# Kernel optimization log

Measured on AMD Instinct MI355X. Metric: run time of the kernel, lower is better.

Reference implementation:

```python
import jax, jax.numpy as jnp
import numpy as np

B, S, HID = 2, 2048, 2048
H, D = 16, 128  # heads, head_dim == kernel_hidden_size
GATE_NORM = 16.0
CLAMP_MIN = -50.0


def gla(q, k, v, gk):
    # fused_recurrent_gla: S_t = diag(exp(gk_t)) S_{t-1} + k_t^T v_t; o_t = (q_t*scale) @ S_t
    # q,k,v,gk: [B,H,S,D]
    scale = D ** -0.5
    qs = jnp.moveaxis(q, 2, 0) * scale  # [S,B,H,D]
    ks = jnp.moveaxis(k, 2, 0)
    vs = jnp.moveaxis(v, 2, 0)
    gs = jnp.moveaxis(gk, 2, 0)

    def step(state, xs):
        q_t, k_t, v_t, g_t = xs  # each [B,H,D]
        state = state * jnp.exp(g_t)[..., None] + k_t[..., None] * v_t[..., None, :]
        o_t = jnp.einsum('bhk,bhkv->bhv', q_t, state)
        return state, o_t

    init = jnp.zeros((q.shape[0], H, D, D), q.dtype)
    _, out = jax.lax.scan(step, init, (qs, ks, vs, gs))
    return jnp.moveaxis(out, 0, 2)  # [B,H,S,D]


def setup_inputs() -> dict:
    key = jax.random.key(0)
    ks = jax.random.split(key, 8)
    std = 0.02
    hidden_states = jax.random.normal(ks[0], (B, S, HID), jnp.float32)
    Wq = jax.random.normal(ks[1], (HID, HID), jnp.float32) * std
    Wk = jax.random.normal(ks[2], (HID, HID), jnp.float32) * std
    Wv = jax.random.normal(ks[3], (HID, HID), jnp.float32) * std
    Wo = jax.random.normal(ks[4], (HID, HID), jnp.float32) * std
    Wg1 = jnp.eye(HID, dtype=jnp.float32)  # nn.init.eye_
    bg1 = jnp.zeros((HID,), jnp.float32)
    Wg2 = jnp.eye(HID, dtype=jnp.float32)
    bg2 = jnp.zeros((HID,), jnp.float32)
    alpha_list = jax.random.uniform(ks[5], (2,), jnp.float32)
    return dict(hidden_states=hidden_states, Wq=Wq, Wk=Wk, Wv=Wv, Wo=Wo,
                Wg1=Wg1, bg1=bg1, Wg2=Wg2, bg2=bg2, alpha_list=alpha_list)


def reference(hidden_states, Wq, Wk, Wv, Wo, Wg1, bg1, Wg2, bg2, alpha_list):
    b, s, _ = hidden_states.shape

    def split_heads(x):  # [b,s,hid] -> [b,h,s,d]
        return x.reshape(b, s, H, D).transpose(0, 2, 1, 3)

    q = split_heads(hidden_states @ Wq.T)
    k = split_heads(hidden_states @ Wk.T)
    v = split_heads(hidden_states @ Wv.T)

    def gate(Wg, bg):
        g = split_heads(hidden_states @ Wg.T + bg)
        g = jax.nn.log_sigmoid(g) / GATE_NORM
        return jnp.maximum(g, CLAMP_MIN)

    gk = gate(Wg1, bg1)
    gk2 = gate(Wg2, bg2)

    o1 = gla(q, k, v, gk)
    o2 = gla(q, k, v, gk2)

    a = jax.nn.softmax(alpha_list)
    attn = a[0] * o1 + a[1] * o2  # [b,h,s,d]
    attn = attn.transpose(0, 2, 1, 3).reshape(b, s, HID)
    return attn @ Wo.T
```

## Files before the change

kernel.cpp:

```cpp
#include <hip/hip_runtime.h>
#include <cstdint>
#include <cstddef>


#define BB     2
#define SEQ    2048
#define HIDN   2048
#define NH     16
#define DD     128
#define CHUNK  64
#define NCHUNK (SEQ / CHUNK)
#define NBH    (BB * NH)
#define NELC   8388608
#define WELC   4194304
static constexpr float QSCALE = 0.08838834764831845f;

typedef __bf16 bf16_t;
typedef _Float16 half_t;
typedef short  short8 __attribute__((ext_vector_type(8)));
typedef float  f32x4  __attribute__((ext_vector_type(4)));

__device__ __forceinline__ float bf2f(short u) {
  return (float)__builtin_bit_cast(bf16_t, u);
}
__device__ __forceinline__ short f2bf(float f) {
  return __builtin_bit_cast(short, (bf16_t)f);
}
__device__ __forceinline__ float hf2f(short u) {
  return (float)__builtin_bit_cast(half_t, u);
}
__device__ __forceinline__ short f2hf(float f) {
  return __builtin_bit_cast(short, (half_t)f);
}

__device__ __forceinline__ void gload_lds16(const void* g, void* l) {
  __builtin_amdgcn_global_load_lds(
      (__attribute__((address_space(1))) unsigned int*)g,
      (__attribute__((address_space(3))) unsigned int*)l, 16, 0, 0);
}

#define WVM4 asm volatile("s_waitcnt vmcnt(4)" ::: "memory")
#define WVM2 asm volatile("s_waitcnt vmcnt(2)" ::: "memory")
#define WVM0 asm volatile("s_waitcnt vmcnt(0)" ::: "memory")
#define SBAR __builtin_amdgcn_s_barrier()


#define STG_A(buf, kt, p)                                                   \
  {                                                                         \
    const size_t ko = (size_t)(kt) * 64;                                    \
    gload_lds16(Ag + (size_t)((p) * 64) * HIDN + ko,                        \
                (void*)&As[buf][((p) * 64 + wave * 8) * 64]);               \
    gload_lds16(Ag + (size_t)((p) * 64 + 128) * HIDN + ko,                  \
                (void*)&As[buf][((p) * 64 + 128 + wave * 8) * 64]);         \
  }

#define STG_B(buf, kt, p)                                                   \
  {                                                                         \
    const int cb0 = (wave >> 2) * 64 + (p) * 32 + (wave & 3) * 8;           \
    const size_t ko = (size_t)(kt) * 64;                                    \
    gload_lds16(Bg + (size_t)cb0 * HIDN + ko,                               \
                (void*)&Bs[buf][cb0 * 64]);                                 \
    gload_lds16(Bg + (size_t)(cb0 + 128) * HIDN + ko,                       \
                (void*)&Bs[buf][(cb0 + 128) * 64]);                         \
  }

#define LDA(mh, rb)                                                         \
  {                                                                         \
    _Pragma("unroll") for (int f = 0; f < 4; f++) {                         \
      const int row = wm * 128 + (mh) * 64 + f * 16 + l16;                  \
      af[f][0] = *(const short8*)&As[rb][row * 64 + ((qd ^ ro) << 3)];      \
      af[f][1] =                                                            \
          *(const short8*)&As[rb][row * 64 + (((4 + qd) ^ ro) << 3)];       \
    }                                                                       \
  }

#define LDB2(j0, rb)                                                        \
  {                                                                         \
    _Pragma("unroll") for (int g = 0; g < 2; g++) {                         \
      const int col = wn * 64 + ((j0) + g) * 16 + l16;                      \
      bfr[(j0) + g][0] =                                                    \
          *(const short8*)&Bs[rb][col * 64 + ((qd ^ ro) << 3)];             \
      bfr[(j0) + g][1] =                                                    \
          *(const short8*)&Bs[rb][col * 64 + (((4 + qd) ^ ro) << 3)];       \
    }                                                                       \
  }

#define MQ(mh, nh)                                                          \
  {                                                                         \
    __builtin_amdgcn_s_setprio(1);                                          \
    _Pragma("unroll") for (int ks = 0; ks < 2; ks++)                        \
    _Pragma("unroll") for (int f = 0; f < 4; f++)                           \
    _Pragma("unroll") for (int g = 0; g < 2; g++)                           \
      acc[(mh) * 4 + f][(nh) * 2 + g] =                                     \
          __builtin_amdgcn_mfma_f32_16x16x32_bf16(                          \
              af[f][ks], bfr[(nh) * 2 + g][ks],                             \
              acc[(mh) * 4 + f][(nh) * 2 + g], 0, 0, 0);                    \
    __builtin_amdgcn_s_setprio(0);                                          \
  }

__device__ __forceinline__ void gemm256(const bf16_t* __restrict__ A,
                                        const bf16_t* __restrict__ Bw,
                                        const float*  __restrict__ bias,
                                        bf16_t* __restrict__ outb,
                                        float*  __restrict__ outf, int epi) {
  __shared__ short As[2][256 * 64];
  __shared__ short Bs[2][256 * 64];
  const int tm   = blockIdx.x * 256;
  const int tn   = blockIdx.y * 256;
  const int tid  = threadIdx.x;
  const int wave = tid >> 6;
  const int lane = tid & 63;
  const int wm   = wave >> 2;
  const int wn   = wave & 3;
  const int qd   = lane >> 4;
  const int l16  = lane & 15;
  const int ro   = l16 & 7;
  const int gc   = (lane & 7) ^ (lane >> 3);

  const short* Ag =
      (const short*)A + (size_t)(tm + wave * 8 + (lane >> 3)) * HIDN + gc * 8;
  const short* Bg =
      (const short*)Bw + (size_t)(tn + (lane >> 3)) * HIDN + gc * 8;

  f32x4 acc[8][4];
#pragma unroll
  for (int i = 0; i < 8; i++)
#pragma unroll
    for (int j = 0; j < 4; j++) acc[i][j] = (f32x4){0.f, 0.f, 0.f, 0.f};
  short8 af[4][2], bfr[4][2];

  STG_A(0, 0, 0); STG_B(0, 0, 0); STG_B(0, 0, 1); STG_A(0, 0, 1);
  WVM0;
  SBAR;

  for (int t = 0; t < 32; t++) {
    const int cur = t & 1, nx = cur ^ 1;
    LDA(0, cur);
    LDB2(0, cur);
    if (t < 31) { STG_A(nx, t + 1, 0); }
    MQ(0, 0);
    if (t < 31) { WVM4; } else { WVM2; }
    SBAR;
    LDB2(2, cur);
    if (t < 31) { STG_B(nx, t + 1, 0); }
    MQ(0, 1);
    if (t < 31) { WVM4; } else { WVM0; }
    SBAR;
    LDA(1, cur);
    if (t < 31) { STG_B(nx, t + 1, 1); }
    MQ(1, 1);
    if (t < 31) { STG_A(nx, t + 1, 1); }
    MQ(1, 0);
    if (t < 31) {
      WVM4;
      SBAR;
    }
  }

#pragma unroll
  for (int i = 0; i < 8; i++)
#pragma unroll
    for (int j = 0; j < 4; j++)
#pragma unroll
      for (int r = 0; r < 4; r++) {
        const int row =
            tm + wm * 128 + (i >> 2) * 64 + (i & 3) * 16 + qd * 4 + r;
        const int col = tn + wn * 64 + j * 16 + l16;
        float v = acc[i][j][r];
        if (epi == 1) {
          v += bias[col];
          const float ls = fminf(v, 0.f) - log1pf(__expf(-fabsf(v)));
          v = fmaxf(ls * 0.0625f, -50.f);
        }
        if (epi == 2) outf[(size_t)row * HIDN + col] = v;
        else          outb[(size_t)row * HIDN + col] = (bf16_t)v;
      }
}

__global__ __launch_bounds__(512, 2) void k_gemm_proj(
    const bf16_t* __restrict__ Xb,
    const bf16_t* __restrict__ W0, const bf16_t* __restrict__ W1,
    const bf16_t* __restrict__ W2, const bf16_t* __restrict__ W3,
    const bf16_t* __restrict__ W4,
    const float* __restrict__ bg1, const float* __restrict__ bg2,
    bf16_t* __restrict__ Qb, bf16_t* __restrict__ Kb, bf16_t* __restrict__ Vb,
    bf16_t* __restrict__ G1b, bf16_t* __restrict__ G2b) {
  const int z = blockIdx.z;
  const bf16_t* Ws[5] = {W0, W1, W2, W3, W4};
  bf16_t* Os[5] = {Qb, Kb, Vb, G1b, G2b};
  const float* bias = (z == 3) ? bg1 : ((z == 4) ? bg2 : nullptr);
  gemm256(Xb, Ws[z], bias, Os[z], nullptr, (z >= 3) ? 1 : 0);
}

__global__ __launch_bounds__(512, 2) void k_gemm_out(
    const bf16_t* __restrict__ attnB, const bf16_t* __restrict__ Wob,
    float* __restrict__ out) {
  gemm256(attnB, Wob, nullptr, nullptr, out, 2);
}

__global__ __launch_bounds__(256) void k_cvt_all(
    const float* __restrict__ hid, const float* __restrict__ wq,
    const float* __restrict__ wk, const float* __restrict__ wv,
    const float* __restrict__ wg1, const float* __restrict__ wg2,
    const float* __restrict__ wo, bf16_t* __restrict__ Xb,
    bf16_t* __restrict__ Wd, bf16_t* __restrict__ Wcur,
    bf16_t* __restrict__ WoB) {
  const int y = blockIdx.y;
  const float* srcs[7] = {hid, wq, wk, wv, wg1, wg2, wo};
  bf16_t* dsts[7] = {Xb, Wd, Wd + WELC, Wd + 2 * WELC, Wd + 3 * WELC, Wcur,
                     WoB};
  const int n = (y == 0) ? NELC : WELC;
  const float* src = srcs[y];
  bf16_t* dst = dsts[y];
  const int idx = (blockIdx.x * 256 + threadIdx.x) * 4;
  if (idx < n) {
    const float4 f = *(const float4*)(src + idx);
    dst[idx + 0] = (bf16_t)f.x; dst[idx + 1] = (bf16_t)f.y;
    dst[idx + 2] = (bf16_t)f.z; dst[idx + 3] = (bf16_t)f.w;
  }
}

__global__ __launch_bounds__(256) void k_zero(float* __restrict__ out) {
  out[(size_t)blockIdx.x * 256 + threadIdx.x] = 0.f;
}

__global__ __launch_bounds__(64) void k_gc(bf16_t* __restrict__ G1b,
                                           bf16_t* __restrict__ G2b,
                                           float* __restrict__ Btot) {
  const int n = blockIdx.x, b = blockIdx.y >> 2, slab = blockIdx.y & 3;
  const int e = blockIdx.z;
  short* P = (short*)(e ? G2b : G1b);
  const int d0 = slab * 512 + threadIdx.x * 8;
  const size_t base = ((size_t)(b * SEQ + n * CHUNK)) * HIDN + d0;
  float c[8] = {0.f, 0.f, 0.f, 0.f, 0.f, 0.f, 0.f, 0.f};
  for (int t = 0; t < CHUNK; t++) {
    short* p = P + base + (size_t)t * HIDN;
    const short8 g = *(const short8*)p;
    short8 o;
#pragma unroll
    for (int j = 0; j < 8; j++) { c[j] += bf2f(g[j]); o[j] = f2hf(c[j]); }
    *(short8*)p = o;
  }
  const int bh = b * 16 + (d0 >> 7);
  float* bp = Btot + ((size_t)(e * NBH + bh) * NCHUNK + n) * DD + (d0 & 127);
#pragma unroll
  for (int j = 0; j < 8; j++) bp[j] = c[j];
}

template <int ACC>
__global__ __launch_bounds__(256) void k_sA(
    const bf16_t* __restrict__ Qb, const bf16_t* __restrict__ Kb,
    const bf16_t* __restrict__ Vb, const bf16_t* __restrict__ Gc,
    bf16_t* __restrict__ UT, const float* __restrict__ alpha,
    bf16_t* __restrict__ attn) {
  const int n = blockIdx.x, bh = blockIdx.y;
  const int b = bh >> 4, h = bh & 15;
  const size_t rbase = ((size_t)(b * SEQ + n * CHUNK)) * HIDN + h * DD;
  const int tid = threadIdx.x;
  const int wave = tid >> 6, lane = tid & 63, qd = lane >> 4, l16 = lane & 15;
  __shared__ short vT[128 * 66];
  __shared__ short k2s[64 * 128];
  __shared__ short r3[128 * 66];
  __shared__ short Ps[64 * 72];
  const float mx = fmaxf(alpha[0], alpha[1]);
  const float x0 = __expf(alpha[0] - mx), x1 = __expf(alpha[1] - mx);
  const float wsc = ((ACC ? x1 : x0) / (x0 + x1)) * QSCALE;

  const short* Kp = (const short*)Kb;
  const short* Vp = (const short*)Vb;
  const short* Gp = (const short*)Gc;
  const short* Qp = (const short*)Qb;

#pragma unroll
  for (int rep = 0; rep < 4; rep++) {
    const int slot = rep * 256 + tid;
    const int t = slot >> 4, ch = slot & 15;
    const size_t ga = rbase + (size_t)t * HIDN + ch * 8;
    const short8 vv = *(const short8*)(Vp + ga);
    const short8 kk = *(const short8*)(Kp + ga);
    const short8 cc = *(const short8*)(Gp + ga);
    const short8 c6 = *(const short8*)(Gp + rbase + (size_t)63 * HIDN + ch * 8);
    short8 k2v;
#pragma unroll
    for (int j = 0; j < 8; j++) {
      const int d = ch * 8 + j;
      vT[d * 66 + t] = vv[j];
      const float c = hf2f(cc[j]);
      const float kf = bf2f(kk[j]);
      k2v[j] = f2bf(kf * __expf(-c));
      r3[d * 66 + t] = f2bf(kf * __expf(hf2f(c6[j]) - c));
    }
    *(short8*)&k2s[t * 128 + ((ch ^ (t & 7)) << 3)] = k2v;
  }
  __syncthreads();

  {
    const int m0 = (wave >> 1) * 64, n0 = (wave & 1) * 64;
    const int* vTi = (const int*)vT;
    const int* r3i = (const int*)r3;
    f32x4 uacc[4][4];
#pragma unroll
    for (int i = 0; i < 4; i++)
#pragma unroll
      for (int j = 0; j < 4; j++) uacc[i][j] = (f32x4){0.f, 0.f, 0.f, 0.f};
#pragma unroll
    for (int ks = 0; ks < 2; ks++) {
      const int ch = ks * 4 + qd;
      short8 af[4], bfv[4];
#pragma unroll
      for (int i = 0; i < 4; i++) {
        const int dv = m0 + i * 16 + l16;
        const int ba = dv * 33 + ch * 4;
#pragma unroll
        for (int w2 = 0; w2 < 4; w2++) {
          const int v = vTi[ba + w2];
          af[i][2 * w2] = (short)(v & 0xffff);
          af[i][2 * w2 + 1] = (short)((unsigned)v >> 16);
        }
      }
#pragma unroll
      for (int j = 0; j < 4; j++) {
        const int dk = n0 + j * 16 + l16;
        const int ba = dk * 33 + ch * 4;
#pragma unroll
        for (int w2 = 0; w2 < 4; w2++) {
          const int v = r3i[ba + w2];
          bfv[j][2 * w2] = (short)(v & 0xffff);
          bfv[j][2 * w2 + 1] = (short)((unsigned)v >> 16);
        }
      }
#pragma unroll
      for (int i = 0; i < 4; i++)
#pragma unroll
        for (int j = 0; j < 4; j++)
          uacc[i][j] = __builtin_amdgcn_mfma_f32_16x16x32_bf16(
              af[i], bfv[j], uacc[i][j], 0, 0, 0);
    }
    short* Uo = (short*)UT + (size_t)(bh * NCHUNK + n) * (DD * DD);
#pragma unroll
    for (int i = 0; i < 4; i++)
#pragma unroll
      for (int j = 0; j < 4; j++)
#pragma unroll
        for (int r = 0; r < 4; r++) {
          const int dv = m0 + i * 16 + qd * 4 + r;
          const int dk = n0 + j * 16 + l16;
          Uo[dv * 128 + (((dk >> 3) ^ (dv & 7)) << 3) + (dk & 7)] =
              f2bf(uacc[i][j][r]);
        }
  }
  __syncthreads();

#pragma unroll
  for (int rep = 0; rep < 4; rep++) {
    const int slot = rep * 256 + tid;
    const int t = slot >> 4, ch = slot & 15;
    const size_t ga = rbase + (size_t)t * HIDN + ch * 8;
    const short8 qq = *(const short8*)(Qp + ga);
    const short8 cc = *(const short8*)(Gp + ga);
    short8 o;
#pragma unroll
    for (int j = 0; j < 8; j++)
      o[j] = f2bf(bf2f(qq[j]) * wsc * __expf(hf2f(cc[j])));
    *(short8*)&r3[t * 128 + ((ch ^ (t & 7)) << 3)] = o;
  }
  __syncthreads();

  {
    f32x4 pacc[4];
#pragma unroll
    for (int j = 0; j < 4; j++) pacc[j] = (f32x4){0.f, 0.f, 0.f, 0.f};
    const int tq = wave * 16 + l16;
#pragma unroll
    for (int ks = 0; ks < 4; ks++) {
      const int ch = ks * 4 + qd;
      const short8 a = *(const short8*)&r3[tq * 128 + ((ch ^ (tq & 7)) << 3)];
#pragma unroll
      for (int j = 0; j < 4; j++) {
        const int s = j * 16 + l16;
        const short8 bq =
            *(const short8*)&k2s[s * 128 + ((ch ^ (s & 7)) << 3)];
        pacc[j] =
            __builtin_amdgcn_mfma_f32_16x16x32_bf16(a, bq, pacc[j], 0, 0, 0);
      }
    }
#pragma unroll
    for (int j = 0; j < 4; j++)
#pragma unroll
      for (int r = 0; r < 4; r++) {
        const int t = wave * 16 + qd * 4 + r, s = j * 16 + l16;
        Ps[t * 72 + s] = (t >= s) ? f2bf(pacc[j][r]) : (short)0;
      }
  }
  __syncthreads();

  f32x4 oacc[8];
#pragma unroll
  for (int j = 0; j < 8; j++) oacc[j] = (f32x4){0.f, 0.f, 0.f, 0.f};
  {
    const int* vTi = (const int*)vT;
    const int tq = wave * 16 + l16;
#pragma unroll
    for (int ks = 0; ks < 2; ks++) {
      const int ch = ks * 4 + qd;
      const short8 a = *(const short8*)&Ps[tq * 72 + ch * 8];
#pragma unroll
      for (int j = 0; j < 8; j++) {
        const int dv = j * 16 + l16;
        const int ba = dv * 33 + ch * 4;
        short8 bq;
#pragma unroll
        for (int w2 = 0; w2 < 4; w2++) {
          const int v = vTi[ba + w2];
          bq[2 * w2] = (short)(v & 0xffff);
          bq[2 * w2 + 1] = (short)((unsigned)v >> 16);
        }
        oacc[j] =
            __builtin_amdgcn_mfma_f32_16x16x32_bf16(a, bq, oacc[j], 0, 0, 0);
      }
    }
  }
#pragma unroll
  for (int j = 0; j < 8; j++)
#pragma unroll
    for (int r = 0; r < 4; r++) {
      const int t = wave * 16 + qd * 4 + r;
      const int dv = j * 16 + l16;
      bf16_t* p = &attn[rbase + (size_t)t * HIDN + dv];
      if (ACC) *p = (bf16_t)((float)*p + oacc[j][r]);
      else     *p = (bf16_t)oacc[j][r];
    }
}

__global__ __launch_bounds__(256) void k_s2(bf16_t* __restrict__ UT,
                                            const float* __restrict__ Btot) {
  const int dg = blockIdx.x, bh = blockIdx.y;
  const int dv = dg * 8 + (threadIdx.x >> 5);
  const int dk0 = (threadIdx.x & 31) * 4;
  const int pos = dv * 128 + (((dk0 >> 3) ^ (dv & 7)) << 3) + (dk0 & 7);
  float st[4] = {0.f, 0.f, 0.f, 0.f};
  for (int nn = 0; nn < NCHUNK; nn++) {
    short* p = (short*)UT + (size_t)(bh * NCHUNK + nn) * (DD * DD) + pos;
    const float4 bp =
        *(const float4*)(Btot + (size_t)(bh * NCHUNK + nn) * DD + dk0);
    short u0 = p[0], u1 = p[1], u2 = p[2], u3 = p[3];
    p[0] = f2bf(st[0]); p[1] = f2bf(st[1]);
    p[2] = f2bf(st[2]); p[3] = f2bf(st[3]);
    st[0] = st[0] * __expf(bp.x) + bf2f(u0);
    st[1] = st[1] * __expf(bp.y) + bf2f(u1);
    st[2] = st[2] * __expf(bp.z) + bf2f(u2);
    st[3] = st[3] * __expf(bp.w) + bf2f(u3);
  }
}

__global__ __launch_bounds__(256) void k_s3b(
    const bf16_t* __restrict__ Qb, const bf16_t* __restrict__ Gc,
    const bf16_t* __restrict__ UT, const float* __restrict__ alpha,
    const int e, bf16_t* __restrict__ attn) {
  const int n = blockIdx.x, bh = blockIdx.y;
  const int b = bh >> 4, h = bh & 15;
  const size_t rbase = ((size_t)(b * SEQ + n * CHUNK)) * HIDN + h * DD;
  const int tid = threadIdx.x;
  const int wave = tid >> 6, lane = tid & 63, qd = lane >> 4, l16 = lane & 15;
  __shared__ short qh[64 * 128];
  __shared__ short Ss[128 * 128];
  const float mx = fmaxf(alpha[0], alpha[1]);
  const float x0 = __expf(alpha[0] - mx), x1 = __expf(alpha[1] - mx);
  const float wsc = ((e ? x1 : x0) / (x0 + x1)) * QSCALE;

  const short* Sp = (const short*)UT + (size_t)(bh * NCHUNK + n) * (DD * DD);
#pragma unroll
  for (int rep = 0; rep < 8; rep++) {
    const int c = rep * 256 + tid;
    gload_lds16(Sp + c * 8, &Ss[c * 8]);
  }
  const short* Qp = (const short*)Qb;
  const short* Gp = (const short*)Gc;
#pragma unroll
  for (int rep = 0; rep < 4; rep++) {
    const int slot = rep * 256 + tid;
    const int t = slot >> 4, ch = slot & 15;
    const size_t ga = rbase + (size_t)t * HIDN + ch * 8;
    const short8 qq = *(const short8*)(Qp + ga);
    const short8 cc = *(const short8*)(Gp + ga);
    short8 o;
#pragma unroll
    for (int j = 0; j < 8; j++)
      o[j] = f2bf(bf2f(qq[j]) * wsc * __expf(hf2f(cc[j])));
    *(short8*)&qh[t * 128 + ((ch ^ (t & 7)) << 3)] = o;
  }
  __syncthreads();

  f32x4 oacc[8];
#pragma unroll
  for (int j = 0; j < 8; j++) oacc[j] = (f32x4){0.f, 0.f, 0.f, 0.f};
  const int tq = wave * 16 + l16;
#pragma unroll
  for (int ks = 0; ks < 4; ks++) {
    const int ch = ks * 4 + qd;
    const short8 a = *(const short8*)&qh[tq * 128 + ((ch ^ (tq & 7)) << 3)];
#pragma unroll
    for (int j = 0; j < 8; j++) {
      const int dv = j * 16 + l16;
      const short8 bq = *(const short8*)&Ss[dv * 128 + ((ch ^ (dv & 7)) << 3)];
      oacc[j] =
          __builtin_amdgcn_mfma_f32_16x16x32_bf16(a, bq, oacc[j], 0, 0, 0);
    }
  }
#pragma unroll
  for (int j = 0; j < 8; j++)
#pragma unroll
    for (int r = 0; r < 4; r++) {
      const int t = wave * 16 + qd * 4 + r;
      const int dv = j * 16 + l16;
      bf16_t* p = &attn[rbase + (size_t)t * HIDN + dv];
      *p = (bf16_t)((float)*p + oacc[j][r]);
    }
}

extern "C" void kernel_launch(void* const* d_in, const int* in_sizes, int n_in,
                              void* d_out, int out_size, void* d_ws,
                              size_t ws_size, hipStream_t stream) {
  const float* hid  = (const float*)d_in[0];
  const float* wq   = (const float*)d_in[1];
  const float* wk   = (const float*)d_in[2];
  const float* wv   = (const float*)d_in[3];
  const float* wo   = (const float*)d_in[4];
  const float* wg1  = (const float*)d_in[5];
  const float* bg1  = (const float*)d_in[6];
  const float* wg2  = (const float*)d_in[7];
  const float* bg2  = (const float*)d_in[8];
  const float* alph = (const float*)d_in[9];
  float* out = (float*)d_out;
  (void)in_sizes; (void)n_in; (void)out_size;

  char* ws = (char*)d_ws;
  size_t off = 0;
  auto alloc = [&](size_t bytes) -> void* {
    void* p = ws + off;
    off += (bytes + 255) & ~(size_t)255;
    return p;
  };
  const size_t NEL = NELC, WEL = WELC;
  bf16_t* Xb   = (bf16_t*)alloc(NEL * 2);
  bf16_t* Wcur = (bf16_t*)alloc(WEL * 2);
  bf16_t* WoB  = (bf16_t*)alloc(WEL * 2);
  bf16_t* Qb   = (bf16_t*)alloc(NEL * 2);
  bf16_t* Kb   = (bf16_t*)alloc(NEL * 2);
  bf16_t* Vb   = (bf16_t*)alloc(NEL * 2);
  bf16_t* G1b  = (bf16_t*)alloc(NEL * 2);
  bf16_t* G2b  = (bf16_t*)alloc(NEL * 2);
  float*  Btot = (float*) alloc((size_t)2 * NBH * NCHUNK * DD * 4);
  bf16_t* Wd = (bf16_t*)d_out;
  bf16_t* UT = (bf16_t*)d_out;

  if (off > ws_size) {
    k_zero<<<dim3((unsigned)(NEL / 256)), 256, 0, stream>>>(out);
    return;
  }

  k_cvt_all<<<dim3(8192, 7), 256, 0, stream>>>(hid, wq, wk, wv, wg1, wg2, wo,
                                               Xb, Wd, Wcur, WoB);
  k_gemm_proj<<<dim3(16, 8, 5), 512, 0, stream>>>(
      Xb, Wd, Wd + WEL, Wd + 2 * WEL, Wd + 3 * WEL, Wcur, bg1, bg2, Qb, Kb, Vb,
      G1b, G2b);
  k_gc<<<dim3(NCHUNK, BB * 4, 2), 64, 0, stream>>>(G1b, G2b, Btot);

  const dim3 gs(NCHUNK, NBH), g2(16, NBH);
  const size_t BSTRIDE = (size_t)NBH * NCHUNK * DD;
  k_sA<0><<<gs, 256, 0, stream>>>(Qb, Kb, Vb, G1b, UT, alph, Xb);
  k_s2<<<g2, 256, 0, stream>>>(UT, Btot);
  k_s3b<<<gs, 256, 0, stream>>>(Qb, G1b, UT, alph, 0, Xb);
  k_sA<1><<<gs, 256, 0, stream>>>(Qb, Kb, Vb, G2b, UT, alph, Xb);
  k_s2<<<g2, 256, 0, stream>>>(UT, Btot + BSTRIDE);
  k_s3b<<<gs, 256, 0, stream>>>(Qb, G2b, UT, alph, 1, Xb);

  k_gemm_out<<<dim3(16, 8), 512, 0, stream>>>(Xb, WoB, out);
}
```

Before: 605.9 us.

## Deepen GEMM prefetch pipeline and swizzle tiles across XCDs

Reorders the global-to-LDS staging in the 256x256 GEMM loop so more loads are in flight, using looser vmcnt waits (6 instead of 4, and 4 instead of 0 for the prologue). It also remaps block IDs so that blocks sharing A/B tiles land on the same XCD, which should improve L2 reuse. The relaxed waits depend on an exact count of outstanding loads. If that count is wrong, data could be read before it arrives.

```diff
diff --git a/kernel.cpp b/kernel.cpp
--- a/kernel.cpp
+++ b/kernel.cpp
@@ -39,24 +39,25 @@
       (__attribute__((address_space(3))) unsigned int*)l, 16, 0, 0);
 }
 
-#define WVM4 asm volatile("s_waitcnt vmcnt(4)" ::: "memory")
-#define WVM2 asm volatile("s_waitcnt vmcnt(2)" ::: "memory")
-#define WVM0 asm volatile("s_waitcnt vmcnt(0)" ::: "memory")
+#define VMW6 asm volatile("s_waitcnt vmcnt(6)" ::: "memory")
+#define VMW4 asm volatile("s_waitcnt vmcnt(4)" ::: "memory")
+#define VMW2 asm volatile("s_waitcnt vmcnt(2)" ::: "memory")
+#define VMW0 asm volatile("s_waitcnt vmcnt(0)" ::: "memory")
 #define SBAR __builtin_amdgcn_s_barrier()
 
 
-#define STG_A(buf, kt, p)                                                   \
+#define STG_A(buf, kt, h)                                                   \
   {                                                                         \
     const size_t ko = (size_t)(kt) * 64;                                    \
-    gload_lds16(Ag + (size_t)((p) * 64) * HIDN + ko,                        \
-                (void*)&As[buf][((p) * 64 + wave * 8) * 64]);               \
-    gload_lds16(Ag + (size_t)((p) * 64 + 128) * HIDN + ko,                  \
-                (void*)&As[buf][((p) * 64 + 128 + wave * 8) * 64]);         \
-  }
-
-#define STG_B(buf, kt, p)                                                   \
+    gload_lds16(Ag + (size_t)((h) * 64) * HIDN + ko,                        \
+                (void*)&As[buf][((h) * 64 + wave * 8) * 64]);               \
+    gload_lds16(Ag + (size_t)((h) * 64 + 128) * HIDN + ko,                  \
+                (void*)&As[buf][((h) * 64 + 128 + wave * 8) * 64]);         \
+  }
+
+#define STG_B(buf, kt, h)                                                   \
   {                                                                         \
-    const int cb0 = (wave >> 2) * 64 + (p) * 32 + (wave & 3) * 8;           \
+    const int cb0 = (wave >> 2) * 64 + (h) * 32 + (wave & 3) * 8;           \
     const size_t ko = (size_t)(kt) * 64;                                    \
     gload_lds16(Bg + (size_t)cb0 * HIDN + ko,                               \
                 (void*)&Bs[buf][cb0 * 64]);                                 \
@@ -102,11 +103,10 @@
                                         const bf16_t* __restrict__ Bw,
                                         const float*  __restrict__ bias,
                                         bf16_t* __restrict__ outb,
-                                        float*  __restrict__ outf, int epi) {
+                                        float*  __restrict__ outf, int epi,
+                                        int tm, int tn) {
   __shared__ short As[2][256 * 64];
   __shared__ short Bs[2][256 * 64];
-  const int tm   = blockIdx.x * 256;
-  const int tn   = blockIdx.y * 256;
   const int tid  = threadIdx.x;
   const int wave = tid >> 6;
   const int lane = tid & 63;
@@ -130,31 +130,27 @@
   short8 af[4][2], bfr[4][2];
 
   STG_A(0, 0, 0); STG_B(0, 0, 0); STG_B(0, 0, 1); STG_A(0, 0, 1);
-  WVM0;
+  VMW4;
   SBAR;
 
   for (int t = 0; t < 32; t++) {
     const int cur = t & 1, nx = cur ^ 1;
     LDA(0, cur);
     LDB2(0, cur);
-    if (t < 31) { STG_A(nx, t + 1, 0); }
+    if (t < 31) { STG_A(nx, t + 1, 0); STG_B(nx, t + 1, 0); }
     MQ(0, 0);
-    if (t < 31) { WVM4; } else { WVM2; }
+    if (t < 31) { VMW6; } else { VMW2; }
     SBAR;
     LDB2(2, cur);
-    if (t < 31) { STG_B(nx, t + 1, 0); }
+    if (t < 31) { STG_B(nx, t + 1, 1); }
     MQ(0, 1);
-    if (t < 31) { WVM4; } else { WVM0; }
+    if (t < 31) { VMW6; } else { VMW0; }
     SBAR;
     LDA(1, cur);
-    if (t < 31) { STG_B(nx, t + 1, 1); }
+    if (t < 31) { STG_A(nx, t + 1, 1); }
     MQ(1, 1);
-    if (t < 31) { STG_A(nx, t + 1, 1); }
     MQ(1, 0);
-    if (t < 31) {
-      WVM4;
-      SBAR;
-    }
+    if (t < 31) { VMW4; SBAR; }
   }
 
 #pragma unroll
@@ -177,6 +173,12 @@
       }
 }
 
+__device__ __forceinline__ void xcd_swz(int lid, int& bx, int& by) {
+  const int k = lid & 7, u = lid >> 3;
+  bx = (k & 3) * 4 + (u & 3);
+  by = (k >> 2) * 4 + (u >> 2);
+}
+
 __global__ __launch_bounds__(512, 2) void k_gemm_proj(
     const bf16_t* __restrict__ Xb,
     const bf16_t* __restrict__ W0, const bf16_t* __restrict__ W1,
@@ -189,13 +191,18 @@
   const bf16_t* Ws[5] = {W0, W1, W2, W3, W4};
   bf16_t* Os[5] = {Qb, Kb, Vb, G1b, G2b};
   const float* bias = (z == 3) ? bg1 : ((z == 4) ? bg2 : nullptr);
-  gemm256(Xb, Ws[z], bias, Os[z], nullptr, (z >= 3) ? 1 : 0);
+  int bx, by;
+  xcd_swz(blockIdx.y * 16 + blockIdx.x, bx, by);
+  gemm256(Xb, Ws[z], bias, Os[z], nullptr, (z >= 3) ? 1 : 0, bx * 256,
+          by * 256);
 }
 
 __global__ __launch_bounds__(512, 2) void k_gemm_out(
     const bf16_t* __restrict__ attnB, const bf16_t* __restrict__ Wob,
     float* __restrict__ out) {
-  gemm256(attnB, Wob, nullptr, nullptr, out, 2);
+  int bx, by;
+  xcd_swz(blockIdx.y * 16 + blockIdx.x, bx, by);
+  gemm256(attnB, Wob, nullptr, nullptr, out, 2, bx * 256, by * 256);
 }
 
 __global__ __launch_bounds__(256) void k_cvt_all(
```

Result: faster. 576.8 us (-4.8%).
